# Kernel optimization log

Measured on AMD Instinct MI355X. Metric: run time of the kernel, lower is better.

## Reference

```python
import jax, jax.numpy as jnp
import numpy as np

EMB = 1024
HEADS = 16
HEAD_DIM = EMB // HEADS


def setup_inputs() -> dict:
    key = jax.random.key(0)
    ks = jax.random.split(key, 9)
    B, T = 2, 2048
    s = 1.0 / np.sqrt(EMB)
    x = jax.random.normal(ks[0], (B, T, EMB), dtype=jnp.float32)
    Wq = jax.random.normal(ks[1], (EMB, EMB), dtype=jnp.float32) * s
    bq = jnp.zeros((EMB,), dtype=jnp.float32)
    Wk = jax.random.normal(ks[2], (EMB, EMB), dtype=jnp.float32) * s
    bk = jnp.zeros((EMB,), dtype=jnp.float32)
    Wv = jax.random.normal(ks[3], (EMB, EMB), dtype=jnp.float32) * s
    bv = jnp.zeros((EMB,), dtype=jnp.float32)
    Wo = jax.random.normal(ks[4], (EMB, EMB), dtype=jnp.float32) * s
    bo = jnp.zeros((EMB,), dtype=jnp.float32)
    return {"x": x, "Wq": Wq, "bq": bq, "Wk": Wk, "bk": bk,
            "Wv": Wv, "bv": bv, "Wo": Wo, "bo": bo}


def reference(x, Wq, bq, Wk, bk, Wv, bv, Wo, bo):
    B, T, C = x.shape
    H, D = HEADS, HEAD_DIM
    # QKV projections -> (B, H, T, D)
    q = (x @ Wq + bq).reshape(B, T, H, D).transpose(0, 2, 1, 3)
    k = (x @ Wk + bk).reshape(B, T, H, D).transpose(0, 2, 1, 3)
    v = (x @ Wv + bv).reshape(B, T, H, D).transpose(0, 2, 1, 3)
    scores = jnp.einsum('bhqd,bhkd->bhqk', q, k) / np.sqrt(D).astype(np.float32)
    causal = jnp.tril(jnp.ones((T, T), dtype=bool))  # True where allowed
    scores = jnp.where(causal, scores, -jnp.inf)
    weights = jax.nn.softmax(scores, axis=-1)  # dropout is identity at eval
    out = jnp.einsum('bhqk,bhkd->bhqd', weights, v)
    out = out.transpose(0, 2, 1, 3).reshape(B, T, C)
    return out @ Wo + bo
```

## Files before the change

kernel.cpp:

```cpp
#include <hip/hip_runtime.h>

typedef unsigned short u16;
typedef u16 u16x8 __attribute__((ext_vector_type(8)));
typedef __bf16 bf16x8 __attribute__((ext_vector_type(8)));
typedef float f32x4 __attribute__((ext_vector_type(4)));

#define EMB 1024
#define TT 2048
#define BB 2
#define NHEADS 16
#define HD 64
#define MTOT (BB * TT)

__device__ __forceinline__ u16 cvt(float f) {
  return __builtin_bit_cast(u16, (__bf16)f);
}

__device__ __forceinline__ bf16x8 asbf(u16x8 v) {
  return __builtin_bit_cast(bf16x8, v);
}

__device__ __forceinline__ void gload16(const void* g, void* l) {
  __builtin_amdgcn_global_load_lds(
      (const __attribute__((address_space(1))) void*)g,
      (__attribute__((address_space(3))) void*)l, 16, 0, 0);
}

__global__ __launch_bounds__(256) void k_prep(
    const float* __restrict__ x, u16* __restrict__ xb,
    const float* __restrict__ W0, const float* __restrict__ W1,
    const float* __restrict__ W2, const float* __restrict__ W3,
    u16* __restrict__ T0, u16* __restrict__ T1, u16* __restrict__ T2,
    u16* __restrict__ T3) {
  __shared__ float tile[32][33];
  const int bid = blockIdx.x;
  const int tid = threadIdx.x;
  if (bid >= 4096) {
    int i = (bid - 4096) * 256 + tid;
    float4 a = ((const float4*)x)[i * 2];
    float4 b = ((const float4*)x)[i * 2 + 1];
    u16x8 o;
    o[0] = cvt(a.x); o[1] = cvt(a.y); o[2] = cvt(a.z); o[3] = cvt(a.w);
    o[4] = cvt(b.x); o[5] = cvt(b.y); o[6] = cvt(b.z); o[7] = cvt(b.w);
    ((u16x8*)xb)[i] = o;
    return;
  }
  const int z = bid >> 10;
  const float* __restrict__ W = (z == 0) ? W0 : (z == 1) ? W1 : (z == 2) ? W2 : W3;
  u16* __restrict__ Wt = (z == 0) ? T0 : (z == 1) ? T1 : (z == 2) ? T2 : T3;
  const int b = bid & 1023;
  const int bx = (b & 31) * 32, by = (b >> 5) * 32;
  const int tx = tid & 31;
  const int ty = tid >> 5;
#pragma unroll
  for (int r = ty; r < 32; r += 8) tile[r][tx] = W[(by + r) * EMB + bx + tx];
  __syncthreads();
#pragma unroll
  for (int r = ty; r < 32; r += 8)
    Wt[(bx + r) * EMB + by + tx] = cvt(tile[tx][r]);
}

__global__ __launch_bounds__(256) void k_gemm_qkv(
    const u16* __restrict__ xb, const u16* __restrict__ WqT,
    const u16* __restrict__ WkT, const u16* __restrict__ WvT,
    const float* __restrict__ bq, const float* __restrict__ bk,
    const float* __restrict__ bv, u16* __restrict__ Q, u16* __restrict__ K,
    u16* __restrict__ Vt) {
  __shared__ u16 Al[128 * 32];
  __shared__ u16 Bl[128 * 32];
  const int tid = threadIdx.x;
  const int lane = tid & 63;
  const int w = tid >> 6;
  const int wr = w >> 1, wc = w & 1;
  const int lr = lane & 15, lg = lane >> 4;
  const int m0 = blockIdx.x * 128;
  const int nb = blockIdx.y;
  const int seg = nb >> 3;
  const int n0 = (nb & 7) * 128;
  const u16* __restrict__ Bt = (seg == 0) ? WqT : (seg == 1) ? WkT : WvT;
  const float* __restrict__ bias = (seg == 0) ? bq : (seg == 1) ? bk : bv;

  f32x4 acc[4][4];
#pragma unroll
  for (int i = 0; i < 4; i++)
#pragma unroll
    for (int j = 0; j < 4; j++) acc[i][j] = (f32x4){0.f, 0.f, 0.f, 0.f};

  const int srow = tid >> 2;
  const int scol = (tid & 3) * 8;
  const u16* ga0 = xb + (m0 + srow) * EMB + scol;
  const u16* gb0 = Bt + (n0 + srow) * EMB + scol;
  char* la0 = (char*)Al + w * 1024;
  char* lb0 = (char*)Bl + w * 1024;

  for (int k0 = 0; k0 < EMB; k0 += 32) {
    gload16(ga0 + k0, la0);
    gload16(ga0 + 64 * EMB + k0, la0 + 4096);
    gload16(gb0 + k0, lb0);
    gload16(gb0 + 64 * EMB + k0, lb0 + 4096);
    __syncthreads();
    u16x8 af[4], bfr[4];
#pragma unroll
    for (int mi = 0; mi < 4; mi++)
      af[mi] = *(const u16x8*)&Al[(wr * 64 + mi * 16 + lr) * 32 + lg * 8];
#pragma unroll
    for (int ni = 0; ni < 4; ni++)
      bfr[ni] = *(const u16x8*)&Bl[(wc * 64 + ni * 16 + lr) * 32 + lg * 8];
#pragma unroll
    for (int mi = 0; mi < 4; mi++)
#pragma unroll
      for (int ni = 0; ni < 4; ni++)
        acc[mi][ni] = __builtin_amdgcn_mfma_f32_16x16x32_bf16(
            asbf(af[mi]), asbf(bfr[ni]), acc[mi][ni], 0, 0, 0);
    __syncthreads();
  }

#pragma unroll
  for (int mi = 0; mi < 4; mi++) {
    const int lmb = wr * 64 + mi * 16 + lg * 4;
#pragma unroll
    for (int ni = 0; ni < 4; ni++) {
      const int ln = wc * 64 + ni * 16 + lr;
      const int n = n0 + ln;
      const float bv_ = bias[n];
      const int h = n >> 6, d = n & 63;
#pragma unroll
      for (int r = 0; r < 4; r++) {
        const int m = m0 + lmb + r;
        const int b = m >> 11, t = m & 2047;
        float v = acc[mi][ni][r] + bv_;
        if (seg == 0) {
          v *= 0.18033688011f;
          Q[(((b * NHEADS + h) * TT) + t) * HD + d] = cvt(v);
        } else if (seg == 1) {
          K[(((b * NHEADS + h) * TT) + t) * HD + d] = cvt(v);
        } else {
          Vt[(((b * NHEADS + h) * HD) + d) * TT + t] = cvt(v);
        }
      }
    }
  }
}

__global__ __launch_bounds__(512) void k_attn(const u16* __restrict__ Q,
                                              const u16* __restrict__ Kg,
                                              const u16* __restrict__ Vt,
                                              u16* __restrict__ AO) {
  __shared__ u16 Kl[2][64 * 64];
  __shared__ u16 Vl[2][64 * 64];
  const int tid = threadIdx.x;
  const int lane = tid & 63;
  const int w = tid >> 6;
  const int lr = lane & 15, lg = lane >> 4;
  const int bh = blockIdx.x;
  const int pair = blockIdx.y;
  const int lo = pair, hi = 31 - pair;
  const int qblk = (w < 4) ? hi : lo;
  const int myend = qblk;
  const int q0 = qblk * 64 + (w & 3) * 16;
  const u16* __restrict__ Qh = Q + bh * TT * HD;
  const u16* __restrict__ Kh = Kg + bh * TT * HD;
  const u16* __restrict__ Vh = Vt + bh * HD * TT;

  const int srow = tid >> 3;
  const int sgz = ((tid >> 3) & 3) | (((tid >> 6) & 1) << 2);
  const int sc = (tid & 7) ^ sgz;

  u16x8 qf[2];
  qf[0] = *(const u16x8*)&Qh[(q0 + lr) * HD + lg * 8];
  qf[1] = *(const u16x8*)&Qh[(q0 + lr) * HD + 32 + lg * 8];

  f32x4 accO[4];
#pragma unroll
  for (int i = 0; i < 4; i++) accO[i] = (f32x4){0.f, 0.f, 0.f, 0.f};
  float mst = -__builtin_inff();
  float lsum = 0.f;

  const int nkt = hi + 1;

  gload16(Kh + srow * HD + sc * 8, (char*)Kl[0] + w * 1024);
  gload16(Vh + srow * TT + sc * 8, (char*)Vl[0] + w * 1024);
  __syncthreads();

  for (int kt = 0; kt < nkt; ++kt) {
    const int k0 = kt * 64;
    const int cur = kt & 1;
    if (kt + 1 < nkt) {
      const int kn = k0 + 64;
      gload16(Kh + (kn + srow) * HD + sc * 8, (char*)Kl[cur ^ 1] + w * 1024);
      gload16(Vh + srow * TT + kn + sc * 8, (char*)Vl[cur ^ 1] + w * 1024);
    }
    if (kt <= myend) {
      const char* Kc = (const char*)Kl[cur];
      const char* Vc = (const char*)Vl[cur];

      f32x4 s[4];
#pragma unroll
      for (int n = 0; n < 4; n++) s[n] = (f32x4){0.f, 0.f, 0.f, 0.f};
      __builtin_amdgcn_s_setprio(1);
#pragma unroll
      for (int n = 0; n < 4; n++) {
        const int kr =
            (lr & 3) + ((n & 1) << 2) + ((lr >> 2) << 3) + ((n >> 1) << 5);
        const int gg = (kr & 3) | (((kr >> 3) & 1) << 2);
#pragma unroll
        for (int dh = 0; dh < 2; dh++) {
          const int bo = ((dh * 4 + lg) ^ gg) << 4;
          u16x8 kf = *(const u16x8*)(Kc + kr * 128 + bo);
          s[n] = __builtin_amdgcn_mfma_f32_16x16x32_bf16(asbf(kf), asbf(qf[dh]),
                                                         s[n], 0, 0, 0);
        }
      }
      __builtin_amdgcn_s_setprio(0);
      if (kt == myend) {
        const int rowq = q0 + lr;
#pragma unroll
        for (int n = 0; n < 4; n++) {
          const int cb = k0 + ((n & 1) << 2) + (lg << 3) + ((n >> 1) << 5);
#pragma unroll
          for (int r = 0; r < 4; r++)
            if (cb + r > rowq) s[n][r] = -__builtin_inff();
        }
      }
      float m01 = fmaxf(fmaxf(s[0][0], s[0][1]), fmaxf(s[0][2], s[0][3]));
      float m1 = fmaxf(fmaxf(s[1][0], s[1][1]), fmaxf(s[1][2], s[1][3]));
      float m2 = fmaxf(fmaxf(s[2][0], s[2][1]), fmaxf(s[2][2], s[2][3]));
      float m3 = fmaxf(fmaxf(s[3][0], s[3][1]), fmaxf(s[3][2], s[3][3]));
      float lmax = fmaxf(fmaxf(m01, m1), fmaxf(m2, m3));
      if (!__all(lmax - mst <= 11.0f)) {
        float rm = lmax;
        rm = fmaxf(rm, __shfl_xor(rm, 16));
        rm = fmaxf(rm, __shfl_xor(rm, 32));
        float mnew = fmaxf(mst, rm);
        float corr = exp2f(mst - mnew);
        lsum *= corr;
        mst = mnew;
#pragma unroll
        for (int r = 0; r < 4; r++) {
          float ca = __shfl(corr, 20 * lg + r);
#pragma unroll
          for (int dt = 0; dt < 4; dt++) accO[dt][r] *= ca;
        }
      }
      float p[4][4];
      float ls = 0.f;
#pragma unroll
      for (int n = 0; n < 4; n++)
#pragma unroll
        for (int r = 0; r < 4; r++) {
          p[n][r] = exp2f(s[n][r] - mst);
          ls += p[n][r];
        }
      lsum += ls;
      u16x8 a1, a2;
#pragma unroll
      for (int r = 0; r < 4; r++) {
        a1[r] = cvt(p[0][r]);
        a1[4 + r] = cvt(p[1][r]);
        a2[r] = cvt(p[2][r]);
        a2[4 + r] = cvt(p[3][r]);
      }
      __builtin_amdgcn_s_setprio(1);
#pragma unroll
      for (int dt = 0; dt < 4; dt++) {
        const int row = dt * 16 + lr;
        const int gg = (row & 3) | (((row >> 3) & 1) << 2);
        const int bo0 = ((lg ^ gg) << 4);
        const int bo1 = (((4 + lg) ^ gg) << 4);
        u16x8 vf0 = *(const u16x8*)(Vc + row * 128 + bo0);
        u16x8 vf1 = *(const u16x8*)(Vc + row * 128 + bo1);
        accO[dt] = __builtin_amdgcn_mfma_f32_16x16x32_bf16(asbf(a1), asbf(vf0),
                                                           accO[dt], 0, 0, 0);
        accO[dt] = __builtin_amdgcn_mfma_f32_16x16x32_bf16(asbf(a2), asbf(vf1),
                                                           accO[dt], 0, 0, 0);
      }
      __builtin_amdgcn_s_setprio(0);
    }
    __syncthreads();
  }
  float t = lsum;
  t += __shfl_xor(t, 16);
  t += __shfl_xor(t, 32);
  float rinv = 1.0f / t;
  float ra[4];
#pragma unroll
  for (int r = 0; r < 4; r++) ra[r] = __shfl(rinv, 20 * lg + r);
  const int b = bh >> 4, h = bh & 15;
#pragma unroll
  for (int dt = 0; dt < 4; dt++)
#pragma unroll
    for (int r = 0; r < 4; r++) {
      const int row = q0 + lg * 4 + r;
      const int d = h * 64 + dt * 16 + lr;
      AO[(b * TT + row) * EMB + d] = cvt(accO[dt][r] * ra[r]);
    }
}

__global__ __launch_bounds__(256) void k_gemm_out(const u16* __restrict__ AO,
                                                  const u16* __restrict__ WoT,
                                                  const float* __restrict__ bo,
                                                  float* __restrict__ out) {
  __shared__ u16 Al[128 * 32];
  __shared__ u16 Bl[128 * 32];
  const int tid = threadIdx.x;
  const int lane = tid & 63;
  const int w = tid >> 6;
  const int wr = w >> 1, wc = w & 1;
  const int lr = lane & 15, lg = lane >> 4;
  const int m0 = blockIdx.x * 128;
  const int n0 = blockIdx.y * 128;

  f32x4 acc[4][4];
#pragma unroll
  for (int i = 0; i < 4; i++)
#pragma unroll
    for (int j = 0; j < 4; j++) acc[i][j] = (f32x4){0.f, 0.f, 0.f, 0.f};

  const int srow = tid >> 2;
  const int scol = (tid & 3) * 8;
  const u16* ga0 = AO + (m0 + srow) * EMB + scol;
  const u16* gb0 = WoT + (n0 + srow) * EMB + scol;
  char* la0 = (char*)Al + w * 1024;
  char* lb0 = (char*)Bl + w * 1024;

  for (int k0 = 0; k0 < EMB; k0 += 32) {
    gload16(ga0 + k0, la0);
    gload16(ga0 + 64 * EMB + k0, la0 + 4096);
    gload16(gb0 + k0, lb0);
    gload16(gb0 + 64 * EMB + k0, lb0 + 4096);
    __syncthreads();
    u16x8 af[4], bfr[4];
#pragma unroll
    for (int mi = 0; mi < 4; mi++)
      af[mi] = *(const u16x8*)&Al[(wr * 64 + mi * 16 + lr) * 32 + lg * 8];
#pragma unroll
    for (int ni = 0; ni < 4; ni++)
      bfr[ni] = *(const u16x8*)&Bl[(wc * 64 + ni * 16 + lr) * 32 + lg * 8];
#pragma unroll
    for (int mi = 0; mi < 4; mi++)
#pragma unroll
      for (int ni = 0; ni < 4; ni++)
        acc[mi][ni] = __builtin_amdgcn_mfma_f32_16x16x32_bf16(
            asbf(af[mi]), asbf(bfr[ni]), acc[mi][ni], 0, 0, 0);
    __syncthreads();
  }

#pragma unroll
  for (int mi = 0; mi < 4; mi++) {
    const int lmb = wr * 64 + mi * 16 + lg * 4;
#pragma unroll
    for (int ni = 0; ni < 4; ni++) {
      const int ln = wc * 64 + ni * 16 + lr;
      const int n = n0 + ln;
      const float bv_ = bo[n];
#pragma unroll
      for (int r = 0; r < 4; r++) {
        const int m = m0 + lmb + r;
        out[m * EMB + n] = acc[mi][ni][r] + bv_;
      }
    }
  }
}

extern "C" void kernel_launch(void* const* d_in, const int* in_sizes, int n_in,
                              void* d_out, int out_size, void* d_ws,
                              size_t ws_size, hipStream_t stream) {
  const float* x = (const float*)d_in[0];
  const float* Wq = (const float*)d_in[1];
  const float* bq = (const float*)d_in[2];
  const float* Wk = (const float*)d_in[3];
  const float* bk = (const float*)d_in[4];
  const float* Wv = (const float*)d_in[5];
  const float* bv = (const float*)d_in[6];
  const float* Wo = (const float*)d_in[7];
  const float* bo = (const float*)d_in[8];
  float* out = (float*)d_out;

  char* ws = (char*)d_ws;
  u16* xb = (u16*)ws;
  u16* WqT = (u16*)(ws + (8u << 20));
  u16* WkT = (u16*)(ws + (10u << 20));
  u16* WvT = (u16*)(ws + (12u << 20));
  u16* WoT = (u16*)(ws + (14u << 20));
  u16* Qb = (u16*)(ws + (16u << 20));
  u16* Kb = (u16*)(ws + (24u << 20));
  u16* Vtb = (u16*)(ws + (32u << 20));
  u16* AO = xb;

  k_prep<<<6144, 256, 0, stream>>>(x, xb, Wq, Wk, Wv, Wo, WqT, WkT, WvT, WoT);
  k_gemm_qkv<<<dim3(32, 24), 256, 0, stream>>>(xb, WqT, WkT, WvT, bq, bk, bv,
                                               Qb, Kb, Vtb);
  k_attn<<<dim3(32, 16), 512, 0, stream>>>(Qb, Kb, Vtb, AO);
  k_gemm_out<<<dim3(32, 8), 256, 0, stream>>>(AO, WoT, bo, out);
}
```

Measured before the change: 114.7 us.

## Deepen GEMM K-tiles with swizzled LDS, split attention into smaller blocks

The QKV and output GEMMs now stage 64-wide K slices per iteration instead of 32, using an XOR-swizzled LDS layout. This halves the number of barriers and main-loop iterations and is meant to avoid LDS bank conflicts. The attention kernel moves from 512-thread blocks pairing 64-row query blocks to 256-thread blocks pairing 32-row query blocks, doubling the grid for better load balance. The weight transpose now writes two bf16 values per 32-bit store. The larger LDS footprint may reduce GEMM occupancy.

Measured after the change: 130.4 us. 1.14x slower.

```diff
diff --git a/kernel.cpp b/kernel.cpp
--- a/kernel.cpp
+++ b/kernel.cpp
@@ -55,9 +55,14 @@
 #pragma unroll
   for (int r = ty; r < 32; r += 8) tile[r][tx] = W[(by + r) * EMB + bx + tx];
   __syncthreads();
-#pragma unroll
-  for (int r = ty; r < 32; r += 8)
-    Wt[(bx + r) * EMB + by + tx] = cvt(tile[tx][r]);
+  const int tx2 = tid & 15;
+  const int ty2 = tid >> 4;
+#pragma unroll
+  for (int r = ty2; r < 32; r += 16) {
+    unsigned v = (unsigned)cvt(tile[2 * tx2][r]) |
+                 ((unsigned)cvt(tile[2 * tx2 + 1][r]) << 16);
+    *(unsigned*)&Wt[(bx + r) * EMB + by + 2 * tx2] = v;
+  }
 }
 
 __global__ __launch_bounds__(256) void k_gemm_qkv(
@@ -66,8 +71,8 @@
     const float* __restrict__ bq, const float* __restrict__ bk,
     const float* __restrict__ bv, u16* __restrict__ Q, u16* __restrict__ K,
     u16* __restrict__ Vt) {
-  __shared__ u16 Al[128 * 32];
-  __shared__ u16 Bl[128 * 32];
+  __shared__ u16 Al[128 * 64];
+  __shared__ u16 Bl[128 * 64];
   const int tid = threadIdx.x;
   const int lane = tid & 63;
   const int w = tid >> 6;
@@ -86,32 +91,43 @@
 #pragma unroll
     for (int j = 0; j < 4; j++) acc[i][j] = (f32x4){0.f, 0.f, 0.f, 0.f};
 
-  const int srow = tid >> 2;
-  const int scol = (tid & 3) * 8;
-  const u16* ga0 = xb + (m0 + srow) * EMB + scol;
-  const u16* gb0 = Bt + (n0 + srow) * EMB + scol;
+  const int srow = tid >> 3;
+  const int sgz = ((tid >> 3) & 3) | (((tid >> 6) & 1) << 2);
+  const int sc = (tid & 7) ^ sgz;
+  const u16* ga0 = xb + (m0 + srow) * EMB + sc * 8;
+  const u16* gb0 = Bt + (n0 + srow) * EMB + sc * 8;
   char* la0 = (char*)Al + w * 1024;
   char* lb0 = (char*)Bl + w * 1024;
-
-  for (int k0 = 0; k0 < EMB; k0 += 32) {
-    gload16(ga0 + k0, la0);
-    gload16(ga0 + 64 * EMB + k0, la0 + 4096);
-    gload16(gb0 + k0, lb0);
-    gload16(gb0 + 64 * EMB + k0, lb0 + 4096);
+  const int gfr = (lr & 3) | (((lr >> 3) & 1) << 2);
+
+  for (int k0 = 0; k0 < EMB; k0 += 64) {
+#pragma unroll
+    for (int m = 0; m < 4; m++) {
+      gload16(ga0 + (32 * m) * EMB + k0, la0 + m * 4096);
+      gload16(gb0 + (32 * m) * EMB + k0, lb0 + m * 4096);
+    }
     __syncthreads();
-    u16x8 af[4], bfr[4];
-#pragma unroll
-    for (int mi = 0; mi < 4; mi++)
-      af[mi] = *(const u16x8*)&Al[(wr * 64 + mi * 16 + lr) * 32 + lg * 8];
-#pragma unroll
-    for (int ni = 0; ni < 4; ni++)
-      bfr[ni] = *(const u16x8*)&Bl[(wc * 64 + ni * 16 + lr) * 32 + lg * 8];
-#pragma unroll
-    for (int mi = 0; mi < 4; mi++)
+    u16x8 af[4][2], bfr[4][2];
+#pragma unroll
+    for (int hh = 0; hh < 2; hh++) {
+      const int pc = ((hh * 4 + lg) ^ gfr) * 16;
+#pragma unroll
+      for (int mi = 0; mi < 4; mi++)
+        af[mi][hh] =
+            *(const u16x8*)((char*)Al + (wr * 64 + mi * 16 + lr) * 128 + pc);
 #pragma unroll
       for (int ni = 0; ni < 4; ni++)
-        acc[mi][ni] = __builtin_amdgcn_mfma_f32_16x16x32_bf16(
-            asbf(af[mi]), asbf(bfr[ni]), acc[mi][ni], 0, 0, 0);
+        bfr[ni][hh] =
+            *(const u16x8*)((char*)Bl + (wc * 64 + ni * 16 + lr) * 128 + pc);
+    }
+#pragma unroll
+    for (int hh = 0; hh < 2; hh++)
+#pragma unroll
+      for (int mi = 0; mi < 4; mi++)
+#pragma unroll
+        for (int ni = 0; ni < 4; ni++)
+          acc[mi][ni] = __builtin_amdgcn_mfma_f32_16x16x32_bf16(
+              asbf(af[mi][hh]), asbf(bfr[ni][hh]), acc[mi][ni], 0, 0, 0);
     __syncthreads();
   }
 
@@ -142,7 +158,7 @@
   }
 }
 
-__global__ __launch_bounds__(512) void k_attn(const u16* __restrict__ Q,
+__global__ __launch_bounds__(256) void k_attn(const u16* __restrict__ Q,
                                               const u16* __restrict__ Kg,
                                               const u16* __restrict__ Vt,
                                               u16* __restrict__ AO) {
@@ -154,10 +170,10 @@
   const int lr = lane & 15, lg = lane >> 4;
   const int bh = blockIdx.x;
   const int pair = blockIdx.y;
-  const int lo = pair, hi = 31 - pair;
-  const int qblk = (w < 4) ? hi : lo;
-  const int myend = qblk;
-  const int q0 = qblk * 64 + (w & 3) * 16;
+  const int lo = pair, hi = 63 - pair;
+  const int b32 = (w < 2) ? hi : lo;
+  const int myend = b32 >> 1;
+  const int q0 = b32 * 32 + (w & 1) * 16;
   const u16* __restrict__ Qh = Q + bh * TT * HD;
   const u16* __restrict__ Kh = Kg + bh * TT * HD;
   const u16* __restrict__ Vh = Vt + bh * HD * TT;
@@ -176,10 +192,12 @@
   float mst = -__builtin_inff();
   float lsum = 0.f;
 
-  const int nkt = hi + 1;
+  const int nkt = (hi >> 1) + 1;
 
   gload16(Kh + srow * HD + sc * 8, (char*)Kl[0] + w * 1024);
+  gload16(Kh + (srow + 32) * HD + sc * 8, (char*)Kl[0] + w * 1024 + 4096);
   gload16(Vh + srow * TT + sc * 8, (char*)Vl[0] + w * 1024);
+  gload16(Vh + (srow + 32) * TT + sc * 8, (char*)Vl[0] + w * 1024 + 4096);
   __syncthreads();
 
   for (int kt = 0; kt < nkt; ++kt) {
@@ -187,8 +205,12 @@
     const int cur = kt & 1;
     if (kt + 1 < nkt) {
       const int kn = k0 + 64;
-      gload16(Kh + (kn + srow) * HD + sc * 8, (char*)Kl[cur ^ 1] + w * 1024);
-      gload16(Vh + srow * TT + kn + sc * 8, (char*)Vl[cur ^ 1] + w * 1024);
+      char* kd = (char*)Kl[cur ^ 1] + w * 1024;
+      char* vd = (char*)Vl[cur ^ 1] + w * 1024;
+      gload16(Kh + (kn + srow) * HD + sc * 8, kd);
+      gload16(Kh + (kn + srow + 32) * HD + sc * 8, kd + 4096);
+      gload16(Vh + srow * TT + kn + sc * 8, vd);
+      gload16(Vh + (srow + 32) * TT + kn + sc * 8, vd + 4096);
     }
     if (kt <= myend) {
       const char* Kc = (const char*)Kl[cur];
@@ -300,8 +322,8 @@
                                                   const u16* __restrict__ WoT,
                                                   const float* __restrict__ bo,
                                                   float* __restrict__ out) {
-  __shared__ u16 Al[128 * 32];
-  __shared__ u16 Bl[128 * 32];
+  __shared__ u16 Al[128 * 64];
+  __shared__ u16 Bl[128 * 64];
   const int tid = threadIdx.x;
   const int lane = tid & 63;
   const int w = tid >> 6;
@@ -316,32 +338,43 @@
 #pragma unroll
     for (int j = 0; j < 4; j++) acc[i][j] = (f32x4){0.f, 0.f, 0.f, 0.f};
 
-  const int srow = tid >> 2;
-  const int scol = (tid & 3) * 8;
-  const u16* ga0 = AO + (m0 + srow) * EMB + scol;
-  const u16* gb0 = WoT + (n0 + srow) * EMB + scol;
+  const int srow = tid >> 3;
+  const int sgz = ((tid >> 3) & 3) | (((tid >> 6) & 1) << 2);
+  const int sc = (tid & 7) ^ sgz;
+  const u16* ga0 = AO + (m0 + srow) * EMB + sc * 8;
+  const u16* gb0 = WoT + (n0 + srow) * EMB + sc * 8;
   char* la0 = (char*)Al + w * 1024;
   char* lb0 = (char*)Bl + w * 1024;
-
-  for (int k0 = 0; k0 < EMB; k0 += 32) {
-    gload16(ga0 + k0, la0);
-    gload16(ga0 + 64 * EMB + k0, la0 + 4096);
-    gload16(gb0 + k0, lb0);
-    gload16(gb0 + 64 * EMB + k0, lb0 + 4096);
+  const int gfr = (lr & 3) | (((lr >> 3) & 1) << 2);
+
+  for (int k0 = 0; k0 < EMB; k0 += 64) {
+#pragma unroll
+    for (int m = 0; m < 4; m++) {
+      gload16(ga0 + (32 * m) * EMB + k0, la0 + m * 4096);
+      gload16(gb0 + (32 * m) * EMB + k0, lb0 + m * 4096);
+    }
     __syncthreads();
-    u16x8 af[4], bfr[4];
-#pragma unroll
-    for (int mi = 0; mi < 4; mi++)
-      af[mi] = *(const u16x8*)&Al[(wr * 64 + mi * 16 + lr) * 32 + lg * 8];
-#pragma unroll
-    for (int ni = 0; ni < 4; ni++)
-      bfr[ni] = *(const u16x8*)&Bl[(wc * 64 + ni * 16 + lr) * 32 + lg * 8];
-#pragma unroll
-    for (int mi = 0; mi < 4; mi++)
+    u16x8 af[4][2], bfr[4][2];
+#pragma unroll
+    for (int hh = 0; hh < 2; hh++) {
+      const int pc = ((hh * 4 + lg) ^ gfr) * 16;
+#pragma unroll
+      for (int mi = 0; mi < 4; mi++)
+        af[mi][hh] =
+            *(const u16x8*)((char*)Al + (wr * 64 + mi * 16 + lr) * 128 + pc);
 #pragma unroll
       for (int ni = 0; ni < 4; ni++)
-        acc[mi][ni] = __builtin_amdgcn_mfma_f32_16x16x32_bf16(
-            asbf(af[mi]), asbf(bfr[ni]), acc[mi][ni], 0, 0, 0);
+        bfr[ni][hh] =
+            *(const u16x8*)((char*)Bl + (wc * 64 + ni * 16 + lr) * 128 + pc);
+    }
+#pragma unroll
+    for (int hh = 0; hh < 2; hh++)
+#pragma unroll
+      for (int mi = 0; mi < 4; mi++)
+#pragma unroll
+        for (int ni = 0; ni < 4; ni++)
+          acc[mi][ni] = __builtin_amdgcn_mfma_f32_16x16x32_bf16(
+              asbf(af[mi][hh]), asbf(bfr[ni][hh]), acc[mi][ni], 0, 0, 0);
     __syncthreads();
   }
 
@@ -390,6 +423,6 @@
   k_prep<<<6144, 256, 0, stream>>>(x, xb, Wq, Wk, Wv, Wo, WqT, WkT, WvT, WoT);
   k_gemm_qkv<<<dim3(32, 24), 256, 0, stream>>>(xb, WqT, WkT, WvT, bq, bk, bv,
                                                Qb, Kb, Vtb);
-  k_attn<<<dim3(32, 16), 512, 0, stream>>>(Qb, Kb, Vtb, AO);
+  k_attn<<<dim3(32, 32), 256, 0, stream>>>(Qb, Kb, Vtb, AO);
   k_gemm_out<<<dim3(32, 8), 256, 0, stream>>>(AO, WoT, bo, out);
 }
```
